# Kernel tuning notes

Measured on AMD Instinct MI355X. Metric: run time of the kernel, lower is better.

The kernel has to match this reference:

```python
import jax, jax.numpy as jnp
import numpy as np

N_NODES = 100000
N_EDGES = 600000
D = 128
H = 256


def setup_inputs() -> dict:
    key = jax.random.key(0)
    ks = jax.random.split(key, 8)
    nodes = jax.random.normal(ks[0], (N_NODES, D), dtype=jnp.float32)
    senders = jax.random.randint(ks[1], (N_EDGES,), 0, N_NODES)
    receivers = jax.random.randint(ks[2], (N_EDGES,), 0, N_NODES)
    s = 0.05
    return {
        "nodes": nodes,
        "senders": senders,
        "receivers": receivers,
        "Wm1": jax.random.normal(ks[3], (D, H), dtype=jnp.float32) * s,
        "bm1": jnp.zeros((H,), dtype=jnp.float32),
        "Wm2": jax.random.normal(ks[4], (H, D), dtype=jnp.float32) * s,
        "bm2": jnp.zeros((D,), dtype=jnp.float32),
        "Wn1": jax.random.normal(ks[5], (2 * D, H), dtype=jnp.float32) * s,
        "bn1": jnp.zeros((H,), dtype=jnp.float32),
        "Wn2": jax.random.normal(ks[6], (H, D), dtype=jnp.float32) * s,
        "bn2": jnp.zeros((D,), dtype=jnp.float32),
    }


def reference(nodes, senders, receivers, Wm1, bm1, Wm2, bm2, Wn1, bn1, Wn2, bn2):
    # message MLP applied per node (vmap(message_fn) over nodes)
    m = jax.nn.relu(nodes @ Wm1 + bm1) @ Wm2 + bm2            # [N, D]
    # gather messages along edges by sender, segment_sum to receivers
    agg = jax.ops.segment_sum(m[senders], receivers, num_segments=nodes.shape[0])  # [N, D]
    # node update MLP on [nodes || aggregated messages]
    h = jnp.concatenate([nodes, agg], axis=-1)                # [N, 2D]
    upd = jax.nn.relu(h @ Wn1 + bn1) @ Wn2 + bn2              # [N, D]
    # residual add
    return nodes + upd
```

## Files before the change

### kernel.cpp

```cpp
#include <hip/hip_runtime.h>
#include <hip/hip_bf16.h>

#define NN 100000
#define DD 128
#define HH 256
#define NE 600000
#define CAP 32

typedef short bf8 __attribute__((ext_vector_type(8)));
typedef float f32x4 __attribute__((ext_vector_type(4)));
typedef unsigned short u16x8 __attribute__((ext_vector_type(8)));

__device__ __forceinline__ unsigned short f2bf(float f) {
  unsigned int u = __builtin_bit_cast(unsigned int, f);
  u += 0x7fffu + ((u >> 16) & 1u);
  return (unsigned short)(u >> 16);
}
__device__ __forceinline__ float bf2f(unsigned short h) {
  unsigned int u = ((unsigned int)h) << 16;
  return __builtin_bit_cast(float, u);
}

__global__ __launch_bounds__(256) void prep(
    const float* __restrict__ Wm1, const float* __restrict__ Wm2,
    const float* __restrict__ Wn1, const float* __restrict__ Wn2,
    unsigned short* __restrict__ Pm1, unsigned short* __restrict__ Pm2,
    unsigned short* __restrict__ Pn1, unsigned short* __restrict__ Pn2,
    int* __restrict__ cnt,
    const float* __restrict__ nodes, unsigned short* __restrict__ Xb) {
  int b = blockIdx.x;
  int gid = b * 256 + threadIdx.x;

  for (int i = gid; i < NN; i += 400 * 256) cnt[i] = 0;

  for (int i = gid; i < NN * DD / 8; i += 400 * 256) {
    const float4 v0 = ((const float4*)nodes)[i * 2];
    const float4 v1 = ((const float4*)nodes)[i * 2 + 1];
    ushort4 o0, o1;
    o0.x = f2bf(v0.x); o0.y = f2bf(v0.y); o0.z = f2bf(v0.z); o0.w = f2bf(v0.w);
    o1.x = f2bf(v1.x); o1.y = f2bf(v1.y); o1.z = f2bf(v1.z); o1.w = f2bf(v1.w);
    ((ushort4*)Xb)[i * 2] = o0;
    ((ushort4*)Xb)[i * 2 + 1] = o1;
  }

  if (b < 80) {
    const float* W; unsigned short* P; int K, N, base;
    if (b < 16)      { W = Wm1; P = Pm1; K = 128; N = 256; base = 0;  }
    else if (b < 32) { W = Wm2; P = Pm2; K = 256; N = 128; base = 16; }
    else if (b < 64) { W = Wn1; P = Pn1; K = 256; N = 256; base = 32; }
    else             { W = Wn2; P = Pn2; K = 256; N = 128; base = 64; }
    int idx = (b - base) * 256 + threadIdx.x;
    int KT = K >> 5;
    int lane = idx & 63;
    int t = idx >> 6;
    int kt = t % KT, nt = t / KT;
    int n = nt * 16 + (lane & 15);
    int k0 = kt * 32 + (lane >> 4) * 8;
    unsigned short* dst = P + (size_t)idx * 8;
#pragma unroll
    for (int j = 0; j < 8; ++j) dst[j] = f2bf(W[(size_t)(k0 + j) * N + n]);
  }
}

__global__ __launch_bounds__(512) void msg_mlp(
    const unsigned short* __restrict__ Xb,
    const unsigned short* __restrict__ W1p, const float* __restrict__ b1,
    const unsigned short* __restrict__ W2p, const float* __restrict__ b2,
    unsigned short* __restrict__ Mb,
    const int* __restrict__ snd, const int* __restrict__ rcv,
    int* __restrict__ cnt, int* __restrict__ ebuf) {
  __shared__ __align__(16) unsigned short h[64][264];
  const int row0 = blockIdx.x * 64;
  const int tid = threadIdx.x;
  const int lane = tid & 63, wave = tid >> 6;
  const int l15 = lane & 15, l4 = lane >> 4;

  {
    int e = blockIdx.x * 512 + tid;
    if (e < NE) {
      int r = rcv[e];
      int pos = atomicAdd(&cnt[r], 1);
      if (pos < CAP) ebuf[r * CAP + pos] = snd[e];
    }
  }

#pragma unroll
  for (int i = 0; i < 2; ++i) {
    int flat = (i * 512 + tid) * 8;
    int r = flat >> 7, c = flat & 127;
    u16x8 v = (u16x8)0;
    if (row0 + r < NN) v = *(const u16x8*)(Xb + (size_t)(row0 + r) * DD + c);
    *(u16x8*)&h[r][c] = v;
  }
  __syncthreads();

  f32x4 acc[2][4];
#pragma unroll
  for (int mt = 0; mt < 2; ++mt)
#pragma unroll
    for (int nt = 0; nt < 4; ++nt) acc[mt][nt] = (f32x4){0.f, 0.f, 0.f, 0.f};
#pragma unroll
  for (int kt = 0; kt < 4; ++kt) {
    bf8 wfr[2], xfr[4];
#pragma unroll
    for (int mt = 0; mt < 2; ++mt) {
      int Htile = wave * 2 + mt;
      wfr[mt] = *(const bf8*)(W1p + ((size_t)(Htile * 4 + kt) * 64 + lane) * 8);
    }
#pragma unroll
    for (int nt = 0; nt < 4; ++nt)
      xfr[nt] = *(const bf8*)&h[nt * 16 + l15][kt * 32 + l4 * 8];
#pragma unroll
    for (int mt = 0; mt < 2; ++mt)
#pragma unroll
      for (int nt = 0; nt < 4; ++nt)
        acc[mt][nt] = __builtin_amdgcn_mfma_f32_16x16x32_bf16(wfr[mt], xfr[nt], acc[mt][nt], 0, 0, 0);
  }
  __syncthreads();

#pragma unroll
  for (int mt = 0; mt < 2; ++mt) {
    int Hbase = wave * 32 + mt * 16 + l4 * 4;
    float4 bv = *(const float4*)(b1 + Hbase);
#pragma unroll
    for (int nt = 0; nt < 4; ++nt) {
      ushort4 o;
      float v0 = acc[mt][nt][0] + bv.x; o.x = f2bf(v0 > 0.f ? v0 : 0.f);
      float v1 = acc[mt][nt][1] + bv.y; o.y = f2bf(v1 > 0.f ? v1 : 0.f);
      float v2 = acc[mt][nt][2] + bv.z; o.z = f2bf(v2 > 0.f ? v2 : 0.f);
      float v3 = acc[mt][nt][3] + bv.w; o.w = f2bf(v3 > 0.f ? v3 : 0.f);
      *(ushort4*)&h[nt * 16 + l15][Hbase] = o;
    }
  }
  __syncthreads();

  f32x4 acc2[4];
#pragma unroll
  for (int nt = 0; nt < 4; ++nt) acc2[nt] = (f32x4){0.f, 0.f, 0.f, 0.f};
#pragma unroll
  for (int kt = 0; kt < 8; ++kt) {
    bf8 wfr, xfr[4];
    wfr = *(const bf8*)(W2p + ((size_t)(wave * 8 + kt) * 64 + lane) * 8);
#pragma unroll
    for (int nt = 0; nt < 4; ++nt)
      xfr[nt] = *(const bf8*)&h[nt * 16 + l15][kt * 32 + l4 * 8];
#pragma unroll
    for (int nt = 0; nt < 4; ++nt)
      acc2[nt] = __builtin_amdgcn_mfma_f32_16x16x32_bf16(wfr, xfr[nt], acc2[nt], 0, 0, 0);
  }
  {
    int Dbase = wave * 16 + l4 * 4;
    float4 bv = *(const float4*)(b2 + Dbase);
#pragma unroll
    for (int nt = 0; nt < 4; ++nt) {
      int node = row0 + nt * 16 + l15;
      if (node < NN) {
        ushort4 o;
        o.x = f2bf(acc2[nt][0] + bv.x);
        o.y = f2bf(acc2[nt][1] + bv.y);
        o.z = f2bf(acc2[nt][2] + bv.z);
        o.w = f2bf(acc2[nt][3] + bv.w);
        *(ushort4*)(Mb + (size_t)node * DD + Dbase) = o;
      }
    }
  }
}

__global__ __launch_bounds__(256) void gather(
    const unsigned short* __restrict__ Mb, const int* __restrict__ ebuf,
    const int* __restrict__ cnt, unsigned short* __restrict__ aggb) {
  int wave = threadIdx.x >> 6;
  int lane = threadIdx.x & 63;
  int half = lane >> 5, sub = lane & 31;
  int node = blockIdx.x * 8 + wave * 2 + half;
  if (node >= NN) return;
  int deg = cnt[node];
  deg = (deg < CAP) ? deg : CAP;
  const int base_e = node * CAP;
  float a0 = 0.f, a1 = 0.f, a2 = 0.f, a3 = 0.f;
  for (int b = 0; b < deg; b += 8) {
    int s[8];
    ushort4 mv[8];
#pragma unroll
    for (int u = 0; u < 8; ++u) s[u] = ebuf[base_e + b + u];
#pragma unroll
    for (int u = 0; u < 8; ++u) {
      int sl = s[u];
      sl = (sl < 0) ? 0 : sl;
      sl = (sl >= NN) ? 0 : sl;
      mv[u] = *(const ushort4*)(Mb + (size_t)sl * DD + sub * 4);
    }
#pragma unroll
    for (int u = 0; u < 8; ++u) {
      bool act = (b + u) < deg;
      a0 += act ? bf2f(mv[u].x) : 0.f;
      a1 += act ? bf2f(mv[u].y) : 0.f;
      a2 += act ? bf2f(mv[u].z) : 0.f;
      a3 += act ? bf2f(mv[u].w) : 0.f;
    }
  }
  ushort4 o;
  o.x = f2bf(a0); o.y = f2bf(a1); o.z = f2bf(a2); o.w = f2bf(a3);
  *(ushort4*)(aggb + (size_t)node * DD + sub * 4) = o;
}

__global__ __launch_bounds__(512) void node_mlp(
    const unsigned short* __restrict__ Xb, const unsigned short* __restrict__ aggb,
    const unsigned short* __restrict__ W1p, const float* __restrict__ b1,
    const unsigned short* __restrict__ W2p, const float* __restrict__ b2,
    float* __restrict__ out) {
  __shared__ __align__(16) unsigned short h[64][264];
  const int row0 = blockIdx.x * 64;
  const int tid = threadIdx.x;
  const int lane = tid & 63, wave = tid >> 6;
  const int l15 = lane & 15, l4 = lane >> 4;

#pragma unroll
  for (int i = 0; i < 2; ++i) {
    int flat = (i * 512 + tid) * 8;
    int r = flat >> 7, c = flat & 127;
    u16x8 v = (u16x8)0;
    if (row0 + r < NN) v = *(const u16x8*)(Xb + (size_t)(row0 + r) * DD + c);
    *(u16x8*)&h[r][c] = v;
  }
#pragma unroll
  for (int i = 0; i < 2; ++i) {
    int flat = (i * 512 + tid) * 8;
    int r = flat >> 7, c = flat & 127;
    u16x8 v = (u16x8)0;
    if (row0 + r < NN) v = *(const u16x8*)(aggb + (size_t)(row0 + r) * DD + c);
    *(u16x8*)&h[r][128 + c] = v;
  }
  __syncthreads();

  ushort4 resid[4];
  {
    int Dbase = wave * 16 + l4 * 4;
#pragma unroll
    for (int nt = 0; nt < 4; ++nt)
      resid[nt] = *(ushort4*)&h[nt * 16 + l15][Dbase];
  }

  f32x4 acc[2][4];
#pragma unroll
  for (int mt = 0; mt < 2; ++mt)
#pragma unroll
    for (int nt = 0; nt < 4; ++nt) acc[mt][nt] = (f32x4){0.f, 0.f, 0.f, 0.f};
#pragma unroll
  for (int kt = 0; kt < 8; ++kt) {
    bf8 wfr[2], xfr[4];
#pragma unroll
    for (int mt = 0; mt < 2; ++mt) {
      int Htile = wave * 2 + mt;
      wfr[mt] = *(const bf8*)(W1p + ((size_t)(Htile * 8 + kt) * 64 + lane) * 8);
    }
#pragma unroll
    for (int nt = 0; nt < 4; ++nt)
      xfr[nt] = *(const bf8*)&h[nt * 16 + l15][kt * 32 + l4 * 8];
#pragma unroll
    for (int mt = 0; mt < 2; ++mt)
#pragma unroll
      for (int nt = 0; nt < 4; ++nt)
        acc[mt][nt] = __builtin_amdgcn_mfma_f32_16x16x32_bf16(wfr[mt], xfr[nt], acc[mt][nt], 0, 0, 0);
  }
  __syncthreads();

#pragma unroll
  for (int mt = 0; mt < 2; ++mt) {
    int Hbase = wave * 32 + mt * 16 + l4 * 4;
    float4 bv = *(const float4*)(b1 + Hbase);
#pragma unroll
    for (int nt = 0; nt < 4; ++nt) {
      ushort4 o;
      float v0 = acc[mt][nt][0] + bv.x; o.x = f2bf(v0 > 0.f ? v0 : 0.f);
      float v1 = acc[mt][nt][1] + bv.y; o.y = f2bf(v1 > 0.f ? v1 : 0.f);
      float v2 = acc[mt][nt][2] + bv.z; o.z = f2bf(v2 > 0.f ? v2 : 0.f);
      float v3 = acc[mt][nt][3] + bv.w; o.w = f2bf(v3 > 0.f ? v3 : 0.f);
      *(ushort4*)&h[nt * 16 + l15][Hbase] = o;
    }
  }
  __syncthreads();

  f32x4 acc2[4];
#pragma unroll
  for (int nt = 0; nt < 4; ++nt) acc2[nt] = (f32x4){0.f, 0.f, 0.f, 0.f};
#pragma unroll
  for (int kt = 0; kt < 8; ++kt) {
    bf8 wfr, xfr[4];
    wfr = *(const bf8*)(W2p + ((size_t)(wave * 8 + kt) * 64 + lane) * 8);
#pragma unroll
    for (int nt = 0; nt < 4; ++nt)
      xfr[nt] = *(const bf8*)&h[nt * 16 + l15][kt * 32 + l4 * 8];
#pragma unroll
    for (int nt = 0; nt < 4; ++nt)
      acc2[nt] = __builtin_amdgcn_mfma_f32_16x16x32_bf16(wfr, xfr[nt], acc2[nt], 0, 0, 0);
  }
  {
    int Dbase = wave * 16 + l4 * 4;
    float4 bv = *(const float4*)(b2 + Dbase);
#pragma unroll
    for (int nt = 0; nt < 4; ++nt) {
      int node = row0 + nt * 16 + l15;
      if (node < NN) {
        float4 o;
        o.x = bf2f(resid[nt].x) + acc2[nt][0] + bv.x;
        o.y = bf2f(resid[nt].y) + acc2[nt][1] + bv.y;
        o.z = bf2f(resid[nt].z) + acc2[nt][2] + bv.z;
        o.w = bf2f(resid[nt].w) + acc2[nt][3] + bv.w;
        *(float4*)(out + (size_t)node * DD + Dbase) = o;
      }
    }
  }
}

extern "C" void kernel_launch(void* const* d_in, const int* in_sizes, int n_in,
                              void* d_out, int out_size, void* d_ws, size_t ws_size,
                              hipStream_t stream) {
  const float* nodes = (const float*)d_in[0];
  const int* senders = (const int*)d_in[1];
  const int* receivers = (const int*)d_in[2];
  const float* Wm1 = (const float*)d_in[3];
  const float* bm1 = (const float*)d_in[4];
  const float* Wm2 = (const float*)d_in[5];
  const float* bm2 = (const float*)d_in[6];
  const float* Wn1 = (const float*)d_in[7];
  const float* bn1 = (const float*)d_in[8];
  const float* Wn2 = (const float*)d_in[9];
  const float* bn2 = (const float*)d_in[10];
  float* out = (float*)d_out;

  char* ws = (char*)d_ws;
  unsigned short* Xb   = (unsigned short*)(ws);
  unsigned short* Mb   = (unsigned short*)(ws + 25600000);
  unsigned short* aggb = (unsigned short*)(ws + 51200000);
  int* cnt    = (int*)(ws + 76800000);
  int* ebuf   = (int*)(ws + 77200000);
  unsigned short* Wm1p = (unsigned short*)(ws + 90000000);
  unsigned short* Wm2p = (unsigned short*)(ws + 90065536);
  unsigned short* Wn1p = (unsigned short*)(ws + 90131072);
  unsigned short* Wn2p = (unsigned short*)(ws + 90262144);

  prep<<<400, 256, 0, stream>>>(Wm1, Wm2, Wn1, Wn2, Wm1p, Wm2p, Wn1p, Wn2p,
                                cnt, nodes, Xb);
  msg_mlp<<<1563, 512, 0, stream>>>(Xb, Wm1p, bm1, Wm2p, bm2, Mb,
                                    senders, receivers, cnt, ebuf);
  gather<<<12500, 256, 0, stream>>>(Mb, ebuf, cnt, aggb);
  node_mlp<<<1563, 512, 0, stream>>>(Xb, aggb, Wn1p, bn1, Wn2p, bn2, out);
}
```

Measured before the change: 240.0 us.

## Fuse gather into node MLP and convert fp32 nodes to bf16 inside MLPs

Removes the separate bf16 copy of the node features. Both MLP kernels now read fp32 nodes and convert them in-register, and the residual is read in full fp32. The gather/segment-sum kernel is folded into the node MLP kernel: each block aggregates the messages for its own 64 nodes directly into shared memory, which removes the aggb round trip and one launch. Count zeroing moves to hipMemsetAsync. The trade-off is more fp32 traffic per MLP tile and longer gather latency inside a heavier 512-thread block, which may reduce latency hiding.

After: 229.6 us. 4.4% less time.

```diff
diff --git a/kernel.cpp b/kernel.cpp
--- a/kernel.cpp
+++ b/kernel.cpp
@@ -1,5 +1,4 @@
 #include <hip/hip_runtime.h>
-#include <hip/hip_bf16.h>
 
 #define NN 100000
 #define DD 128
@@ -21,49 +20,31 @@
   return __builtin_bit_cast(float, u);
 }
 
-__global__ __launch_bounds__(256) void prep(
+__global__ __launch_bounds__(256) void pack(
     const float* __restrict__ Wm1, const float* __restrict__ Wm2,
     const float* __restrict__ Wn1, const float* __restrict__ Wn2,
     unsigned short* __restrict__ Pm1, unsigned short* __restrict__ Pm2,
-    unsigned short* __restrict__ Pn1, unsigned short* __restrict__ Pn2,
-    int* __restrict__ cnt,
-    const float* __restrict__ nodes, unsigned short* __restrict__ Xb) {
+    unsigned short* __restrict__ Pn1, unsigned short* __restrict__ Pn2) {
   int b = blockIdx.x;
-  int gid = b * 256 + threadIdx.x;
-
-  for (int i = gid; i < NN; i += 400 * 256) cnt[i] = 0;
-
-  for (int i = gid; i < NN * DD / 8; i += 400 * 256) {
-    const float4 v0 = ((const float4*)nodes)[i * 2];
-    const float4 v1 = ((const float4*)nodes)[i * 2 + 1];
-    ushort4 o0, o1;
-    o0.x = f2bf(v0.x); o0.y = f2bf(v0.y); o0.z = f2bf(v0.z); o0.w = f2bf(v0.w);
-    o1.x = f2bf(v1.x); o1.y = f2bf(v1.y); o1.z = f2bf(v1.z); o1.w = f2bf(v1.w);
-    ((ushort4*)Xb)[i * 2] = o0;
-    ((ushort4*)Xb)[i * 2 + 1] = o1;
-  }
-
-  if (b < 80) {
-    const float* W; unsigned short* P; int K, N, base;
-    if (b < 16)      { W = Wm1; P = Pm1; K = 128; N = 256; base = 0;  }
-    else if (b < 32) { W = Wm2; P = Pm2; K = 256; N = 128; base = 16; }
-    else if (b < 64) { W = Wn1; P = Pn1; K = 256; N = 256; base = 32; }
-    else             { W = Wn2; P = Pn2; K = 256; N = 128; base = 64; }
-    int idx = (b - base) * 256 + threadIdx.x;
-    int KT = K >> 5;
-    int lane = idx & 63;
-    int t = idx >> 6;
-    int kt = t % KT, nt = t / KT;
-    int n = nt * 16 + (lane & 15);
-    int k0 = kt * 32 + (lane >> 4) * 8;
-    unsigned short* dst = P + (size_t)idx * 8;
-#pragma unroll
-    for (int j = 0; j < 8; ++j) dst[j] = f2bf(W[(size_t)(k0 + j) * N + n]);
-  }
+  const float* W; unsigned short* P; int K, N, base;
+  if (b < 16)      { W = Wm1; P = Pm1; K = 128; N = 256; base = 0;  }
+  else if (b < 32) { W = Wm2; P = Pm2; K = 256; N = 128; base = 16; }
+  else if (b < 64) { W = Wn1; P = Pn1; K = 256; N = 256; base = 32; }
+  else             { W = Wn2; P = Pn2; K = 256; N = 128; base = 64; }
+  int idx = (b - base) * 256 + threadIdx.x;
+  int KT = K >> 5;
+  int lane = idx & 63;
+  int t = idx >> 6;
+  int kt = t % KT, nt = t / KT;
+  int n = nt * 16 + (lane & 15);
+  int k0 = kt * 32 + (lane >> 4) * 8;
+  unsigned short* dst = P + (size_t)idx * 8;
+#pragma unroll
+  for (int j = 0; j < 8; ++j) dst[j] = f2bf(W[(size_t)(k0 + j) * N + n]);
 }
 
 __global__ __launch_bounds__(512) void msg_mlp(
-    const unsigned short* __restrict__ Xb,
+    const float* __restrict__ nodes,
     const unsigned short* __restrict__ W1p, const float* __restrict__ b1,
     const unsigned short* __restrict__ W2p, const float* __restrict__ b2,
     unsigned short* __restrict__ Mb,
@@ -88,9 +69,14 @@
   for (int i = 0; i < 2; ++i) {
     int flat = (i * 512 + tid) * 8;
     int r = flat >> 7, c = flat & 127;
-    u16x8 v = (u16x8)0;
-    if (row0 + r < NN) v = *(const u16x8*)(Xb + (size_t)(row0 + r) * DD + c);
-    *(u16x8*)&h[r][c] = v;
+    u16x8 o = (u16x8)0;
+    if (row0 + r < NN) {
+      const float4 v0 = *(const float4*)(nodes + (size_t)(row0 + r) * DD + c);
+      const float4 v1 = *(const float4*)(nodes + (size_t)(row0 + r) * DD + c + 4);
+      o[0] = f2bf(v0.x); o[1] = f2bf(v0.y); o[2] = f2bf(v0.z); o[3] = f2bf(v0.w);
+      o[4] = f2bf(v1.x); o[5] = f2bf(v1.y); o[6] = f2bf(v1.z); o[7] = f2bf(v1.w);
+    }
+    *(u16x8*)&h[r][c] = o;
   }
   __syncthreads();
 
@@ -166,46 +152,9 @@
   }
 }
 
-__global__ __launch_bounds__(256) void gather(
-    const unsigned short* __restrict__ Mb, const int* __restrict__ ebuf,
-    const int* __restrict__ cnt, unsigned short* __restrict__ aggb) {
-  int wave = threadIdx.x >> 6;
-  int lane = threadIdx.x & 63;
-  int half = lane >> 5, sub = lane & 31;
-  int node = blockIdx.x * 8 + wave * 2 + half;
-  if (node >= NN) return;
-  int deg = cnt[node];
-  deg = (deg < CAP) ? deg : CAP;
-  const int base_e = node * CAP;
-  float a0 = 0.f, a1 = 0.f, a2 = 0.f, a3 = 0.f;
-  for (int b = 0; b < deg; b += 8) {
-    int s[8];
-    ushort4 mv[8];
-#pragma unroll
-    for (int u = 0; u < 8; ++u) s[u] = ebuf[base_e + b + u];
-#pragma unroll
-    for (int u = 0; u < 8; ++u) {
-      int sl = s[u];
-      sl = (sl < 0) ? 0 : sl;
-      sl = (sl >= NN) ? 0 : sl;
-      mv[u] = *(const ushort4*)(Mb + (size_t)sl * DD + sub * 4);
-    }
-#pragma unroll
-    for (int u = 0; u < 8; ++u) {
-      bool act = (b + u) < deg;
-      a0 += act ? bf2f(mv[u].x) : 0.f;
-      a1 += act ? bf2f(mv[u].y) : 0.f;
-      a2 += act ? bf2f(mv[u].z) : 0.f;
-      a3 += act ? bf2f(mv[u].w) : 0.f;
-    }
-  }
-  ushort4 o;
-  o.x = f2bf(a0); o.y = f2bf(a1); o.z = f2bf(a2); o.w = f2bf(a3);
-  *(ushort4*)(aggb + (size_t)node * DD + sub * 4) = o;
-}
-
-__global__ __launch_bounds__(512) void node_mlp(
-    const unsigned short* __restrict__ Xb, const unsigned short* __restrict__ aggb,
+__global__ __launch_bounds__(512) void node_fused(
+    const float* __restrict__ nodes, const unsigned short* __restrict__ Mb,
+    const int* __restrict__ ebuf, const int* __restrict__ cnt,
     const unsigned short* __restrict__ W1p, const float* __restrict__ b1,
     const unsigned short* __restrict__ W2p, const float* __restrict__ b2,
     float* __restrict__ out) {
@@ -214,32 +163,81 @@
   const int tid = threadIdx.x;
   const int lane = tid & 63, wave = tid >> 6;
   const int l15 = lane & 15, l4 = lane >> 4;
+  const int halfid = lane >> 5, sub = lane & 31;
+
+  int degv[4], basev[4], s_all[4][8];
+#pragma unroll
+  for (int t = 0; t < 4; ++t) {
+    int node = row0 + t * 16 + wave * 2 + halfid;
+    basev[t] = node * CAP;
+    int d = (node < NN) ? cnt[node] : 0;
+    degv[t] = d < CAP ? d : CAP;
+  }
+#pragma unroll
+  for (int t = 0; t < 4; ++t)
+#pragma unroll
+    for (int u = 0; u < 8; ++u) s_all[t][u] = ebuf[basev[t] + u];
 
 #pragma unroll
   for (int i = 0; i < 2; ++i) {
     int flat = (i * 512 + tid) * 8;
     int r = flat >> 7, c = flat & 127;
-    u16x8 v = (u16x8)0;
-    if (row0 + r < NN) v = *(const u16x8*)(Xb + (size_t)(row0 + r) * DD + c);
-    *(u16x8*)&h[r][c] = v;
-  }
-#pragma unroll
-  for (int i = 0; i < 2; ++i) {
-    int flat = (i * 512 + tid) * 8;
-    int r = flat >> 7, c = flat & 127;
-    u16x8 v = (u16x8)0;
-    if (row0 + r < NN) v = *(const u16x8*)(aggb + (size_t)(row0 + r) * DD + c);
-    *(u16x8*)&h[r][128 + c] = v;
-  }
-  __syncthreads();
-
-  ushort4 resid[4];
-  {
-    int Dbase = wave * 16 + l4 * 4;
-#pragma unroll
-    for (int nt = 0; nt < 4; ++nt)
-      resid[nt] = *(ushort4*)&h[nt * 16 + l15][Dbase];
-  }
+    u16x8 o = (u16x8)0;
+    if (row0 + r < NN) {
+      const float4 v0 = *(const float4*)(nodes + (size_t)(row0 + r) * DD + c);
+      const float4 v1 = *(const float4*)(nodes + (size_t)(row0 + r) * DD + c + 4);
+      o[0] = f2bf(v0.x); o[1] = f2bf(v0.y); o[2] = f2bf(v0.z); o[3] = f2bf(v0.w);
+      o[4] = f2bf(v1.x); o[5] = f2bf(v1.y); o[6] = f2bf(v1.z); o[7] = f2bf(v1.w);
+    }
+    *(u16x8*)&h[r][c] = o;
+  }
+
+#pragma unroll
+  for (int t = 0; t < 4; ++t) {
+    int ln = t * 16 + wave * 2 + halfid;
+    int deg = degv[t];
+    float a0 = 0.f, a1 = 0.f, a2 = 0.f, a3 = 0.f;
+    {
+      ushort4 mv[8];
+#pragma unroll
+      for (int u = 0; u < 8; ++u) {
+        int sl = s_all[t][u];
+        sl = ((unsigned)sl >= NN) ? 0 : sl;
+        mv[u] = *(const ushort4*)(Mb + (size_t)sl * DD + sub * 4);
+      }
+#pragma unroll
+      for (int u = 0; u < 8; ++u) {
+        bool act = u < deg;
+        a0 += act ? bf2f(mv[u].x) : 0.f;
+        a1 += act ? bf2f(mv[u].y) : 0.f;
+        a2 += act ? bf2f(mv[u].z) : 0.f;
+        a3 += act ? bf2f(mv[u].w) : 0.f;
+      }
+    }
+    for (int bb = 8; bb < deg; bb += 8) {
+      int s[8]; ushort4 mv[8];
+#pragma unroll
+      for (int u = 0; u < 8; ++u) s[u] = ebuf[basev[t] + bb + u];
+#pragma unroll
+      for (int u = 0; u < 8; ++u) {
+        int sl = s[u];
+        sl = ((unsigned)sl >= NN) ? 0 : sl;
+        mv[u] = *(const ushort4*)(Mb + (size_t)sl * DD + sub * 4);
+      }
+#pragma unroll
+      for (int u = 0; u < 8; ++u) {
+        bool act = (bb + u) < deg;
+        a0 += act ? bf2f(mv[u].x) : 0.f;
+        a1 += act ? bf2f(mv[u].y) : 0.f;
+        a2 += act ? bf2f(mv[u].z) : 0.f;
+        a3 += act ? bf2f(mv[u].w) : 0.f;
+      }
+    }
+    ushort4 o;
+    o.x = f2bf(a0); o.y = f2bf(a1); o.z = f2bf(a2); o.w = f2bf(a3);
+    *(ushort4*)&h[ln][128 + sub * 4] = o;
+  }
+  __syncthreads();
 
   f32x4 acc[2][4];
 #pragma unroll
@@ -281,6 +279,15 @@
   }
   __syncthreads();
 
+  const int Dbase = wave * 16 + l4 * 4;
+  float4 rv[4];
+#pragma unroll
+  for (int nt = 0; nt < 4; ++nt) {
+    int node = row0 + nt * 16 + l15;
+    rv[nt] = (node < NN) ? *(const float4*)(nodes + (size_t)node * DD + Dbase)
+                         : (float4){0.f, 0.f, 0.f, 0.f};
+  }
+
   f32x4 acc2[4];
 #pragma unroll
   for (int nt = 0; nt < 4; ++nt) acc2[nt] = (f32x4){0.f, 0.f, 0.f, 0.f};
@@ -296,17 +303,16 @@
       acc2[nt] = __builtin_amdgcn_mfma_f32_16x16x32_bf16(wfr, xfr[nt], acc2[nt], 0, 0, 0);
   }
   {
-    int Dbase = wave * 16 + l4 * 4;
     float4 bv = *(const float4*)(b2 + Dbase);
 #pragma unroll
     for (int nt = 0; nt < 4; ++nt) {
       int node = row0 + nt * 16 + l15;
       if (node < NN) {
         float4 o;
-        o.x = bf2f(resid[nt].x) + acc2[nt][0] + bv.x;
-        o.y = bf2f(resid[nt].y) + acc2[nt][1] + bv.y;
-        o.z = bf2f(resid[nt].z) + acc2[nt][2] + bv.z;
-        o.w = bf2f(resid[nt].w) + acc2[nt][3] + bv.w;
+        o.x = rv[nt].x + acc2[nt][0] + bv.x;
+        o.y = rv[nt].y + acc2[nt][1] + bv.y;
+        o.z = rv[nt].z + acc2[nt][2] + bv.z;
+        o.w = rv[nt].w + acc2[nt][3] + bv.w;
         *(float4*)(out + (size_t)node * DD + Dbase) = o;
       }
     }
@@ -330,20 +336,18 @@
   float* out = (float*)d_out;
 
   char* ws = (char*)d_ws;
-  unsigned short* Xb   = (unsigned short*)(ws);
-  unsigned short* Mb   = (unsigned short*)(ws + 25600000);
-  unsigned short* aggb = (unsigned short*)(ws + 51200000);
-  int* cnt    = (int*)(ws + 76800000);
-  int* ebuf   = (int*)(ws + 77200000);
-  unsigned short* Wm1p = (unsigned short*)(ws + 90000000);
-  unsigned short* Wm2p = (unsigned short*)(ws + 90065536);
-  unsigned short* Wn1p = (unsigned short*)(ws + 90131072);
-  unsigned short* Wn2p = (unsigned short*)(ws + 90262144);
-
-  prep<<<400, 256, 0, stream>>>(Wm1, Wm2, Wn1, Wn2, Wm1p, Wm2p, Wn1p, Wn2p,
-                                cnt, nodes, Xb);
-  msg_mlp<<<1563, 512, 0, stream>>>(Xb, Wm1p, bm1, Wm2p, bm2, Mb,
+  unsigned short* Mb   = (unsigned short*)(ws);
+  int* cnt    = (int*)(ws + 25600000);
+  int* ebuf   = (int*)(ws + 26000000);
+  unsigned short* Wm1p = (unsigned short*)(ws + 38800000);
+  unsigned short* Wm2p = (unsigned short*)(ws + 38865536);
+  unsigned short* Wn1p = (unsigned short*)(ws + 38931072);
+  unsigned short* Wn2p = (unsigned short*)(ws + 39062144);
+
+  hipMemsetAsync(cnt, 0, NN * sizeof(int), stream);
+  pack<<<80, 256, 0, stream>>>(Wm1, Wm2, Wn1, Wn2, Wm1p, Wm2p, Wn1p, Wn2p);
+  msg_mlp<<<1563, 512, 0, stream>>>(nodes, Wm1p, bm1, Wm2p, bm2, Mb,
                                     senders, receivers, cnt, ebuf);
-  gather<<<12500, 256, 0, stream>>>(Mb, ebuf, cnt, aggb);
-  node_mlp<<<1563, 512, 0, stream>>>(Xb, aggb, Wn1p, bn1, Wn2p, bn2, out);
-}
+  node_fused<<<1563, 512, 0, stream>>>(nodes, Mb, ebuf, cnt,
+                                       Wn1p, bn1, Wn2p, bn2, out);
+}
```
